# Optimization experiments

Hardware: AMD Instinct MI355X
Metric: run time of the kernel (lower is better)

The kernel has to match this reference:

```python
import jax, jax.numpy as jnp
import numpy as np

B, N, T, H, P = 512, 128, 336, 32, 1  # batch, nodes, seq_len, hidden, pred_len


def setup_inputs() -> dict:
    key = jax.random.key(0)
    ks = jax.random.split(key, 9)
    s = 1.0 / np.sqrt(H)  # torch LSTM/Linear init bound
    u = lambda k, shape: jax.random.uniform(k, shape, dtype=jnp.float32, minval=-s, maxval=s)
    return {
        "x": jax.random.normal(ks[0], (B, N, T), dtype=jnp.float32),
        # layer 0: input_size=1
        "W_ih0": u(ks[1], (N, 4 * H, 1)),
        "W_hh0": u(ks[2], (N, 4 * H, H)),
        "b0": u(ks[3], (N, 4 * H)),  # = b_ih0 + b_hh0 (additive in the cell)
        # layer 1: input_size=H
        "W_ih1": u(ks[4], (N, 4 * H, H)),
        "W_hh1": u(ks[5], (N, 4 * H, H)),
        "b1": u(ks[6], (N, 4 * H)),
        # per-node linear head
        "W_fc": u(ks[7], (N, P, H)),
        "b_fc": u(ks[8], (N, P)),
    }


def _cell(x_proj, h, c, W_hh, b):
    # x_proj, h, c: [B, N, H*(...)]; torch gate order: i, f, g, o
    gates = x_proj + jnp.einsum("bnh,ngh->bng", h, W_hh) + b
    i, f, g, o = jnp.split(gates, 4, axis=-1)
    c = jax.nn.sigmoid(f) * c + jax.nn.sigmoid(i) * jnp.tanh(g)
    h = jax.nn.sigmoid(o) * jnp.tanh(c)
    return h, c


def reference(x, W_ih0, W_hh0, b0, W_ih1, W_hh1, b1, W_fc, b_fc):
    Bx, Nx, Tx = x.shape
    Hx = W_hh0.shape[-1]
    Wi0 = W_ih0[:, :, 0]  # [N, 4H] since input_size == 1
    xs = jnp.moveaxis(x, 2, 0)  # [T, B, N]
    zeros = jnp.zeros((Bx, Nx, Hx), x.dtype)
    init = (zeros, zeros, zeros, zeros)  # h0, c0, h1, c1

    def step(carry, x_t):
        h0, c0, h1, c1 = carry
        xp0 = x_t[:, :, None] * Wi0[None]          # [B, N, 4H]
        h0, c0 = _cell(xp0, h0, c0, W_hh0, b0)
        xp1 = jnp.einsum("bnh,ngh->bng", h0, W_ih1)
        h1, c1 = _cell(xp1, h1, c1, W_hh1, b1)
        return (h0, c0, h1, c1), None

    (h0, c0, h1, c1), _ = jax.lax.scan(step, init, xs)
    # last-timestep top-layer hidden through per-node linear head
    return jnp.einsum("bnh,nph->bnp", h1, W_fc) + b_fc[None]
```

## Files before the change

### kernel.cpp

```cpp
#include <hip/hip_runtime.h>
#include <stdint.h>

#define NB 512
#define NN 128
#define NT 336
#define NH 32
#define NG 128

typedef short bf16x8 __attribute__((ext_vector_type(8)));
typedef float f32x4  __attribute__((ext_vector_type(4)));
typedef float f32x2  __attribute__((ext_vector_type(2)));
typedef float f32v4  __attribute__((ext_vector_type(4)));

#define LOG2E 1.4426950408889634f

__device__ __forceinline__ f32x2 exp2v(f32x2 v) {
  f32x2 r; r.x = __builtin_amdgcn_exp2f(v.x); r.y = __builtin_amdgcn_exp2f(v.y); return r;
}
__device__ __forceinline__ f32x2 rcpv(f32x2 v) {
  f32x2 r; r.x = __builtin_amdgcn_rcpf(v.x); r.y = __builtin_amdgcn_rcpf(v.y); return r;
}
__device__ __forceinline__ short f2bf(float f) {
  unsigned u = __builtin_bit_cast(unsigned, f) + 0x8000u;
  return (short)(u >> 16);
}

template<bool BIAS>
__device__ __forceinline__ f32x2 cell_pair(f32x2 gi, f32x2 gf, f32x2 gg, f32x2 go,
                                           f32x2& cst, float ebi, float ebf,
                                           float ebg, float ebo) {
  f32x2 wi = exp2v(gi), wf = exp2v(gf), uu = exp2v(gg), wo = exp2v(go);
  f32x2 Ai, Af, Au, Ao, nu;
  if (BIAS) {
    Ai = wi * ebi + 1.0f;
    Af = wf * ebf + 1.0f;
    Au = uu * ebg + 1.0f;
    Ao = wo * ebo + 1.0f;
    nu = 1.0f - uu * ebg;
  } else {
    Ai = wi + 1.0f; Af = wf + 1.0f; Au = uu + 1.0f; Ao = wo + 1.0f;
    nu = 1.0f - uu;
  }
  f32x2 P  = Ai * Au;
  f32x2 N  = cst * P + nu * Af;
  f32x2 cn = N * rcpv(Af * P);
  cst = cn;
  f32x2 sarg = cn * (-2.0f * LOG2E);
  sarg.x = fminf(sarg.x, 80.0f);
  sarg.y = fminf(sarg.y, 80.0f);
  f32x2 vv = exp2v(sarg);
  f32x2 hh = (1.0f - vv) * rcpv(Ao * (vv + 1.0f));
  return hh;
}

__global__ __launch_bounds__(256, 2) void lstm_kernel(
    const float* __restrict__ x,
    const float* __restrict__ Wih0,
    const float* __restrict__ Whh0,
    const float* __restrict__ b0,
    const float* __restrict__ Wih1,
    const float* __restrict__ Whh1,
    const float* __restrict__ b1,
    const float* __restrict__ Wfc,
    const float* __restrict__ bfc,
    float* __restrict__ out)
{
  const int tid  = threadIdx.x;
  const int wave = tid >> 6;
  const int lane = tid & 63;
  const int c    = lane & 15;
  const int q    = lane >> 4;
  const int n    = blockIdx.x >> 3;
  const int m0   = ((blockIdx.x & 7) * 4 + wave) * 16;

  __shared__ short lds[4 * 2 * 16 * 40];
  short* my0 = lds + wave * (2 * 16 * 40);
  short* my1 = my0 + 16 * 40;

  const float sc_tab[8] = {-LOG2E, -LOG2E, -LOG2E, -LOG2E,
                           -2.0f * LOG2E, -2.0f * LOG2E, -LOG2E, -LOG2E};

  bf16x8 wb0[8], wb1[8], wb2[8];
  {
    const float* pW0 = Whh0 + n * (NG * NH);
    const float* pW1 = Wih1 + n * (NG * NH);
    const float* pW2 = Whh1 + n * (NG * NH);
#pragma unroll
    for (int tau = 0; tau < 8; ++tau) {
      int off = (tau * 16 + c) * NH + q * 8;
      float sc = sc_tab[tau];
#pragma unroll
      for (int j = 0; j < 8; ++j) {
        wb0[tau][j] = f2bf(sc * pW0[off + j]);
        wb1[tau][j] = f2bf(sc * pW1[off + j]);
        wb2[tau][j] = f2bf(sc * pW2[off + j]);
      }
    }
  }
  float b0g[8], eb1[8], wi0g[8];
#pragma unroll
  for (int tau = 0; tau < 8; ++tau) {
    int g = tau * 16 + c;
    float sc = sc_tab[tau];
    b0g[tau]  = sc * b0[n * NG + g];
    eb1[tau]  = __builtin_amdgcn_exp2f(sc * b1[n * NG + g]);
    wi0g[tau] = sc * Wih0[n * NG + g];
  }
  const float wfc0 = Wfc[n * NH + c];
  const float wfc1 = Wfc[n * NH + 16 + c];

  const float* px0 = x + ((size_t)(m0 + q * 4 + 0) * NN + n) * NT;
  const float* px1 = x + ((size_t)(m0 + q * 4 + 1) * NN + n) * NT;
  const float* px2 = x + ((size_t)(m0 + q * 4 + 2) * NN + n) * NT;
  const float* px3 = x + ((size_t)(m0 + q * 4 + 3) * NN + n) * NT;

  bf16x8 a0 = {0,0,0,0,0,0,0,0};
  bf16x8 a1 = {0,0,0,0,0,0,0,0};
  f32x2 c0p[2][2], c1p[2][2], h1p[2][2];
#pragma unroll
  for (int tu = 0; tu < 2; ++tu)
#pragma unroll
    for (int p = 0; p < 2; ++p) {
      c0p[tu][p] = (f32x2){0.f, 0.f};
      c1p[tu][p] = (f32x2){0.f, 0.f};
      h1p[tu][p] = (f32x2){0.f, 0.f};
    }

  const f32x4 zero4 = {0.f, 0.f, 0.f, 0.f};

#pragma unroll 1
  for (int t4 = 0; t4 < NT / 4; ++t4) {
    f32v4 xr0 = *(const f32v4*)(px0 + t4 * 4);
    f32v4 xr1 = *(const f32v4*)(px1 + t4 * 4);
    f32v4 xr2 = *(const f32v4*)(px2 + t4 * 4);
    f32v4 xr3 = *(const f32v4*)(px3 + t4 * 4);

#pragma unroll
    for (int ts = 0; ts < 4; ++ts) {
      f32x2 x01 = {xr0[ts], xr1[ts]};
      f32x2 x23 = {xr2[ts], xr3[ts]};

      f32x4 acc[8];
#pragma unroll
      for (int tau = 0; tau < 8; ++tau) {
        f32x2 w2 = {wi0g[tau], wi0g[tau]};
        f32x2 b2 = {b0g[tau], b0g[tau]};
        f32x2 lo = x01 * w2 + b2;
        f32x2 hi = x23 * w2 + b2;
        acc[tau] = (f32x4){lo.x, lo.y, hi.x, hi.y};
      }
#pragma unroll
      for (int tau = 0; tau < 8; ++tau)
        acc[tau] = __builtin_amdgcn_mfma_f32_16x16x32_bf16(a0, wb0[tau], acc[tau], 0, 0, 0);

#pragma unroll
      for (int tu = 0; tu < 2; ++tu) {
#pragma unroll
        for (int p = 0; p < 2; ++p) {
          f32x2 gi = { acc[tu    ][2*p], acc[tu    ][2*p+1] };
          f32x2 gf = { acc[tu + 2][2*p], acc[tu + 2][2*p+1] };
          f32x2 gg = { acc[tu + 4][2*p], acc[tu + 4][2*p+1] };
          f32x2 go = { acc[tu + 6][2*p], acc[tu + 6][2*p+1] };
          f32x2 hh = cell_pair<false>(gi, gf, gg, go, c0p[tu][p], 1.f, 1.f, 1.f, 1.f);
          my0[(q * 4 + 2*p    ) * 40 + tu * 16 + c] = f2bf(hh.x);
          my0[(q * 4 + 2*p + 1) * 40 + tu * 16 + c] = f2bf(hh.y);
        }
      }
      asm volatile("" ::: "memory");
      a0 = *(const bf16x8*)(my0 + c * 40 + q * 8);

#pragma unroll
      for (int tau = 0; tau < 8; ++tau)
        acc[tau] = __builtin_amdgcn_mfma_f32_16x16x32_bf16(a0, wb1[tau], zero4, 0, 0, 0);
#pragma unroll
      for (int tau = 0; tau < 8; ++tau)
        acc[tau] = __builtin_amdgcn_mfma_f32_16x16x32_bf16(a1, wb2[tau], acc[tau], 0, 0, 0);

#pragma unroll
      for (int tu = 0; tu < 2; ++tu) {
#pragma unroll
        for (int p = 0; p < 2; ++p) {
          f32x2 gi = { acc[tu    ][2*p], acc[tu    ][2*p+1] };
          f32x2 gf = { acc[tu + 2][2*p], acc[tu + 2][2*p+1] };
          f32x2 gg = { acc[tu + 4][2*p], acc[tu + 4][2*p+1] };
          f32x2 go = { acc[tu + 6][2*p], acc[tu + 6][2*p+1] };
          f32x2 hh = cell_pair<true>(gi, gf, gg, go, c1p[tu][p],
                                     eb1[tu], eb1[tu + 2], eb1[tu + 4], eb1[tu + 6]);
          h1p[tu][p] = hh;
          my1[(q * 4 + 2*p    ) * 40 + tu * 16 + c] = f2bf(hh.x);
          my1[(q * 4 + 2*p + 1) * 40 + tu * 16 + c] = f2bf(hh.y);
        }
      }
      asm volatile("" ::: "memory");
      a1 = *(const bf16x8*)(my1 + c * 40 + q * 8);
    }
  }

  float s0 = h1p[0][0].x * wfc0 + h1p[1][0].x * wfc1;
  float s1 = h1p[0][0].y * wfc0 + h1p[1][0].y * wfc1;
  float s2 = h1p[0][1].x * wfc0 + h1p[1][1].x * wfc1;
  float s3 = h1p[0][1].y * wfc0 + h1p[1][1].y * wfc1;
#pragma unroll
  for (int off = 1; off < 16; off <<= 1) {
    s0 += __shfl_xor(s0, off, 64);
    s1 += __shfl_xor(s1, off, 64);
    s2 += __shfl_xor(s2, off, 64);
    s3 += __shfl_xor(s3, off, 64);
  }
  if (c < 4) {
    float v = (c == 0) ? s0 : (c == 1) ? s1 : (c == 2) ? s2 : s3;
    out[(size_t)(m0 + q * 4 + c) * NN + n] = v + bfc[n];
  }
}

extern "C" void kernel_launch(void* const* d_in, const int* in_sizes, int n_in,
                              void* d_out, int out_size, void* d_ws, size_t ws_size,
                              hipStream_t stream) {
  const float* x    = (const float*)d_in[0];
  const float* Wih0 = (const float*)d_in[1];
  const float* Whh0 = (const float*)d_in[2];
  const float* b0   = (const float*)d_in[3];
  const float* Wih1 = (const float*)d_in[4];
  const float* Whh1 = (const float*)d_in[5];
  const float* b1   = (const float*)d_in[6];
  const float* Wfc  = (const float*)d_in[7];
  const float* bfc  = (const float*)d_in[8];
  float* out = (float*)d_out;

  lstm_kernel<<<dim3(1024), dim3(256), 0, stream>>>(
      x, Wih0, Whh0, b0, Wih1, Whh1, b1, Wfc, bfc, out);
}
```

Before: 1.295 ms.

## Cut register pressure to raise occupancy to three blocks per CU

```diff
diff --git a/kernel.cpp b/kernel.cpp
--- a/kernel.cpp
+++ b/kernel.cpp
@@ -10,9 +10,9 @@
 typedef short bf16x8 __attribute__((ext_vector_type(8)));
 typedef float f32x4  __attribute__((ext_vector_type(4)));
 typedef float f32x2  __attribute__((ext_vector_type(2)));
-typedef float f32v4  __attribute__((ext_vector_type(4)));
 
 #define LOG2E 1.4426950408889634f
+#define KNEG  (-2.0f * LOG2E)
 
 __device__ __forceinline__ f32x2 exp2v(f32x2 v) {
   f32x2 r; r.x = __builtin_amdgcn_exp2f(v.x); r.y = __builtin_amdgcn_exp2f(v.y); return r;
@@ -28,24 +28,24 @@
 template<bool BIAS>
 __device__ __forceinline__ f32x2 cell_pair(f32x2 gi, f32x2 gf, f32x2 gg, f32x2 go,
                                            f32x2& cst, float ebi, float ebf,
-                                           float ebg, float ebo) {
+                                           float kng, float ebo) {
   f32x2 wi = exp2v(gi), wf = exp2v(gf), uu = exp2v(gg), wo = exp2v(go);
-  f32x2 Ai, Af, Au, Ao, nu;
+  f32x2 Ai, Af, Au, Ao, nuk;
   if (BIAS) {
-    Ai = wi * ebi + 1.0f;
-    Af = wf * ebf + 1.0f;
-    Au = uu * ebg + 1.0f;
-    Ao = wo * ebo + 1.0f;
-    nu = 1.0f - uu * ebg;
+    Ai  = wi * ebi + 1.0f;
+    Af  = wf * ebf + 1.0f;
+    Au  = uu * (kng * (-1.0f / KNEG)) + 1.0f;
+    Ao  = wo * ebo + 1.0f;
+    nuk = uu * kng + KNEG;
   } else {
-    Ai = wi + 1.0f; Af = wf + 1.0f; Au = uu + 1.0f; Ao = wo + 1.0f;
-    nu = 1.0f - uu;
+    Ai  = wi + 1.0f; Af = wf + 1.0f; Au = uu + 1.0f; Ao = wo + 1.0f;
+    nuk = uu * (-KNEG) + KNEG;
   }
   f32x2 P  = Ai * Au;
-  f32x2 N  = cst * P + nu * Af;
-  f32x2 cn = N * rcpv(Af * P);
-  cst = cn;
-  f32x2 sarg = cn * (-2.0f * LOG2E);
+  f32x2 N  = cst * P + nuk * Af;
+  f32x2 cS = N * rcpv(Af * P);
+  cst = cS;
+  f32x2 sarg = cS;
   sarg.x = fminf(sarg.x, 80.0f);
   sarg.y = fminf(sarg.y, 80.0f);
   f32x2 vv = exp2v(sarg);
@@ -53,7 +53,7 @@
   return hh;
 }
 
-__global__ __launch_bounds__(256, 2) void lstm_kernel(
+__global__ __launch_bounds__(256, 3) void lstm_kernel(
     const float* __restrict__ x,
     const float* __restrict__ Wih0,
     const float* __restrict__ Whh0,
@@ -103,7 +103,8 @@
     int g = tau * 16 + c;
     float sc = sc_tab[tau];
     b0g[tau]  = sc * b0[n * NG + g];
-    eb1[tau]  = __builtin_amdgcn_exp2f(sc * b1[n * NG + g]);
+    float e   = __builtin_amdgcn_exp2f(sc * b1[n * NG + g]);
+    eb1[tau]  = (tau == 4 || tau == 5) ? (-KNEG) * e : e;
     wi0g[tau] = sc * Wih0[n * NG + g];
   }
   const float wfc0 = Wfc[n * NH + c];
@@ -116,27 +117,26 @@
 
   bf16x8 a0 = {0,0,0,0,0,0,0,0};
   bf16x8 a1 = {0,0,0,0,0,0,0,0};
-  f32x2 c0p[2][2], c1p[2][2], h1p[2][2];
+  f32x2 c0p[2][2], c1p[2][2];
 #pragma unroll
   for (int tu = 0; tu < 2; ++tu)
 #pragma unroll
     for (int p = 0; p < 2; ++p) {
       c0p[tu][p] = (f32x2){0.f, 0.f};
       c1p[tu][p] = (f32x2){0.f, 0.f};
-      h1p[tu][p] = (f32x2){0.f, 0.f};
     }
 
   const f32x4 zero4 = {0.f, 0.f, 0.f, 0.f};
 
 #pragma unroll 1
-  for (int t4 = 0; t4 < NT / 4; ++t4) {
-    f32v4 xr0 = *(const f32v4*)(px0 + t4 * 4);
-    f32v4 xr1 = *(const f32v4*)(px1 + t4 * 4);
-    f32v4 xr2 = *(const f32v4*)(px2 + t4 * 4);
-    f32v4 xr3 = *(const f32v4*)(px3 + t4 * 4);
-
-#pragma unroll
-    for (int ts = 0; ts < 4; ++ts) {
+  for (int t2 = 0; t2 < NT / 2; ++t2) {
+    f32x2 xr0 = *(const f32x2*)(px0 + t2 * 2);
+    f32x2 xr1 = *(const f32x2*)(px1 + t2 * 2);
+    f32x2 xr2 = *(const f32x2*)(px2 + t2 * 2);
+    f32x2 xr3 = *(const f32x2*)(px3 + t2 * 2);
+
+#pragma unroll
+    for (int ts = 0; ts < 2; ++ts) {
       f32x2 x01 = {xr0[ts], xr1[ts]};
       f32x2 x23 = {xr2[ts], xr3[ts]};
 
@@ -186,7 +186,6 @@
           f32x2 go = { acc[tu + 6][2*p], acc[tu + 6][2*p+1] };
           f32x2 hh = cell_pair<true>(gi, gf, gg, go, c1p[tu][p],
                                      eb1[tu], eb1[tu + 2], eb1[tu + 4], eb1[tu + 6]);
-          h1p[tu][p] = hh;
           my1[(q * 4 + 2*p    ) * 40 + tu * 16 + c] = f2bf(hh.x);
           my1[(q * 4 + 2*p + 1) * 40 + tu * 16 + c] = f2bf(hh.y);
         }
@@ -196,10 +195,18 @@
     }
   }
 
-  float s0 = h1p[0][0].x * wfc0 + h1p[1][0].x * wfc1;
-  float s1 = h1p[0][0].y * wfc0 + h1p[1][0].y * wfc1;
-  float s2 = h1p[0][1].x * wfc0 + h1p[1][1].x * wfc1;
-  float s3 = h1p[0][1].y * wfc0 + h1p[1][1].y * wfc1;
+  float h1v[2][4];
+#pragma unroll
+  for (int tu = 0; tu < 2; ++tu)
+#pragma unroll
+    for (int r = 0; r < 4; ++r) {
+      unsigned short us = (unsigned short)my1[(q * 4 + r) * 40 + tu * 16 + c];
+      h1v[tu][r] = __builtin_bit_cast(float, ((unsigned)us) << 16);
+    }
+  float s0 = h1v[0][0] * wfc0 + h1v[1][0] * wfc1;
+  float s1 = h1v[0][1] * wfc0 + h1v[1][1] * wfc1;
+  float s2 = h1v[0][2] * wfc0 + h1v[1][2] * wfc1;
+  float s3 = h1v[0][3] * wfc0 + h1v[1][3] * wfc1;
 #pragma unroll
   for (int off = 1; off < 16; off <<= 1) {
     s0 += __shfl_xor(s0, off, 64);
```

Result: slower. 4.460 ms (+244.5%).
